# Performance work log

Hardware: AMD Instinct MI355X
Metric: run time of the kernel (lower is better)

## Reference

```python
import jax, jax.numpy as jnp
import numpy as np

B, S, D, E, K = 4, 2048, 2048, 64, 2

def setup_inputs() -> dict:
    key = jax.random.key(0)
    k1, k2, k3, k4 = jax.random.split(key, 4)
    x = jax.random.normal(k1, (B, S, D), dtype=jnp.float32)
    W = jax.random.normal(k2, (E, D), dtype=jnp.float32) * 0.02  # gate_linear.weight
    noise_weight = jax.random.normal(k3, (E,), dtype=jnp.float32) * 0.02
    noise = jax.random.normal(k4, (B, S, E), dtype=jnp.float32)  # torch.randn_like(logits), noisy_std=1.0
    return {"x": x, "W": W, "noise_weight": noise_weight, "noise": noise, "k": K}

def reference(x, W, noise_weight, noise, k):
    # logits = x @ W.T  -> [B, S, E]
    logits = jnp.einsum('bsd,ed->bse', x, W)
    # noise injection: randn * noisy_std(=1.0) * noise_weight (per-expert scale)
    logits_noisy = logits + noise * noise_weight
    # top-k over experts
    top_vals, top_idx = jax.lax.top_k(logits_noisy, k)  # [B, S, k]
    # softmax over a tensor that is -inf everywhere except the top-k slots is
    # exactly: zeros everywhere, softmax(top_vals) scattered into the top-k slots.
    probs = jax.nn.softmax(top_vals, axis=-1)  # [B, S, k]
    n_tok = B * S
    rows = jnp.arange(n_tok)[:, None]  # [n_tok, 1]
    gated = jnp.zeros((n_tok, E), dtype=logits.dtype)
    gated = gated.at[rows, top_idx.reshape(n_tok, k)].set(probs.reshape(n_tok, k))
    gated = gated.reshape(B, S, E)
    return gated, top_idx, top_vals
```

## Files before the change

kernel.cpp:

```cpp
#include <hip/hip_runtime.h>
#include <math.h>

#define NTOK 8192
#define DDIM 2048
#define NEXP 64
#define MT   16
#define BK   256
#define NCH  (DDIM / BK)
#define XSTR 264
#define CSTR 66

typedef _Float16 f16x8 __attribute__((ext_vector_type(8)));
typedef float    f32x4 __attribute__((ext_vector_type(4)));

#define GATED_SZ (NTOK * NEXP)
#define IDX_OFF  GATED_SZ
#define VALS_OFF (GATED_SZ + NTOK * 2)

#define NKSTEP (DDIM / 32)
#define NTILE  (NEXP / 16)
#define BFRAG_HALVES ((size_t)NKSTEP * NTILE * 64 * 8)

__global__ void pack_b_kernel(const float* __restrict__ W,
                              _Float16* __restrict__ Bh,
                              _Float16* __restrict__ Bl)
{
    const int tid  = blockIdx.x * blockDim.x + threadIdx.x;
    const int lane = tid & 63;
    const int fid  = tid >> 6;
    const int ks   = fid >> 2;
    const int nt   = fid & 3;
    const int e    = nt * 16 + (lane & 15);
    const int k    = ks * 32 + (lane >> 4) * 8;
    const float* src = W + (size_t)e * DDIM + k;

    f16x8 hi, lo;
#pragma unroll
    for (int j = 0; j < 8; ++j) {
        const float v = src[j];
        const _Float16 h = (_Float16)v;
        hi[j] = h;
        lo[j] = (_Float16)((v - (float)h) * 4096.f);
    }
    *(f16x8*)(Bh + (size_t)tid * 8) = hi;
    *(f16x8*)(Bl + (size_t)tid * 8) = lo;
}

#define BFRAG(base, ks) (*(const f16x8*)((base) + ((((size_t)(ks)) * 4 + nt) * 64 + lane) * 8))

__global__ __launch_bounds__(512, 4) void gate_kernel(
    const float* __restrict__ x,
    const _Float16* __restrict__ Bh,
    const _Float16* __restrict__ Bl,
    const float* __restrict__ noise_w,
    const float* __restrict__ noise,
    float* __restrict__ out)
{
    __shared__ _Float16 xh[2][MT * XSTR];
    __shared__ _Float16 xl[2][MT * XSTR];
    __shared__ float    cbuf[2][MT * CSTR];

    const int tid  = threadIdx.x;
    const int lane = tid & 63;
    const int w    = __builtin_amdgcn_readfirstlane(tid >> 6);
    const int h    = w >> 2;
    const int nt   = w & 3;
    const int tokBase = blockIdx.x * MT;

    const int srow = tid >> 5;
    const int scol = tid & 31;
    const float* xsrc = x + (size_t)(tokBase + srow) * DDIM + scol * 8;

    const int q = lane >> 4;
    const int m = lane & 15;
    const int abase = m * XSTR + h * (BK / 2) + q * 8;

    f32x4 acc_hh = {0.f, 0.f, 0.f, 0.f};
    f32x4 acc_lo = {0.f, 0.f, 0.f, 0.f};

    float4 st0 = *(const float4*)(xsrc);
    float4 st1 = *(const float4*)(xsrc + 4);

    for (int c = 0; c < NCH; ++c) {
        const int p = c & 1;

        {
            f16x8 h8, l8;
            const float vv[8] = {st0.x, st0.y, st0.z, st0.w,
                                 st1.x, st1.y, st1.z, st1.w};
#pragma unroll
            for (int j = 0; j < 8; ++j) {
                const _Float16 hh = (_Float16)vv[j];
                h8[j] = hh;
                l8[j] = (_Float16)((vv[j] - (float)hh) * 4096.f);
            }
            *(f16x8*)&xh[p][srow * XSTR + scol * 8] = h8;
            *(f16x8*)&xl[p][srow * XSTR + scol * 8] = l8;
        }

        if (c + 1 < NCH) {
            st0 = *(const float4*)(xsrc + (size_t)(c + 1) * BK);
            st1 = *(const float4*)(xsrc + (size_t)(c + 1) * BK + 4);
        }

        __syncthreads();

        const int ksb = c * 8 + h * 4;
#pragma unroll
        for (int stp = 0; stp < 4; ++stp) {
            const f16x8 bh = BFRAG(Bh, ksb + stp);
            const f16x8 bl = BFRAG(Bl, ksb + stp);
            const f16x8 ah = *(const f16x8*)&xh[p][abase + stp * 32];
            const f16x8 al = *(const f16x8*)&xl[p][abase + stp * 32];
            acc_hh = __builtin_amdgcn_mfma_f32_16x16x32_f16(ah, bh, acc_hh, 0, 0, 0);
            acc_lo = __builtin_amdgcn_mfma_f32_16x16x32_f16(ah, bl, acc_lo, 0, 0, 0);
            acc_lo = __builtin_amdgcn_mfma_f32_16x16x32_f16(al, bh, acc_lo, 0, 0, 0);
        }
    }

    {
        const int e = nt * 16 + m;
#pragma unroll
        for (int r = 0; r < 4; ++r) {
            const int t = q * 4 + r;
            cbuf[h][t * CSTR + e] = acc_hh[r] + acc_lo[r] * (1.f / 4096.f);
        }
    }
    __syncthreads();

    const float nwv = noise_w[lane];
#pragma unroll
    for (int i = 0; i < 2; ++i) {
        const int t   = w * 2 + i;
        const int tok = tokBase + t;
        const int e   = lane;

        float v = cbuf[0][t * CSTR + e] + cbuf[1][t * CSTR + e]
                + noise[(size_t)tok * NEXP + e] * nwv;

        float m1 = v; int i1 = e;
#pragma unroll
        for (int sh = 32; sh > 0; sh >>= 1) {
            float ov = __shfl_xor(m1, sh, 64);
            int   oi = __shfl_xor(i1, sh, 64);
            if (ov > m1 || (ov == m1 && oi < i1)) { m1 = ov; i1 = oi; }
        }
        float vm = (e == i1) ? -INFINITY : v;
        float m2 = vm; int i2 = e;
#pragma unroll
        for (int sh = 32; sh > 0; sh >>= 1) {
            float ov = __shfl_xor(m2, sh, 64);
            int   oi = __shfl_xor(i2, sh, 64);
            if (ov > m2 || (ov == m2 && oi < i2)) { m2 = ov; i2 = oi; }
        }

        const float e2  = expf(m2 - m1);
        const float inv = 1.f / (1.f + e2);
        const float p1  = inv;
        const float p2  = e2 * inv;

        float gval = 0.f;
        if (e == i1) gval = p1;
        else if (e == i2) gval = p2;
        out[(size_t)tok * NEXP + e] = gval;

        if (lane == 0) {
            out[IDX_OFF  + tok * 2 + 0] = (float)i1;
            out[IDX_OFF  + tok * 2 + 1] = (float)i2;
            out[VALS_OFF + tok * 2 + 0] = m1;
            out[VALS_OFF + tok * 2 + 1] = m2;
        }
    }
}

extern "C" void kernel_launch(void* const* d_in, const int* in_sizes, int n_in,
                              void* d_out, int out_size, void* d_ws, size_t ws_size,
                              hipStream_t stream) {
    const float* x      = (const float*)d_in[0];
    const float* W      = (const float*)d_in[1];
    const float* nw     = (const float*)d_in[2];
    const float* noise  = (const float*)d_in[3];
    float* out = (float*)d_out;

    _Float16* Bh = (_Float16*)d_ws;
    _Float16* Bl = Bh + BFRAG_HALVES;

    hipLaunchKernelGGL(pack_b_kernel, dim3(64), dim3(256), 0, stream, W, Bh, Bl);

    hipLaunchKernelGGL(gate_kernel, dim3(NTOK / MT), dim3(512), 0, stream,
                       x, Bh, Bl, nw, noise, out);
}
```

Before: 112.5 us.

## Split K across two blocks with atomic-counter reduction of partial logits

Splits the 2048-long reduction across two separate 256-thread blocks per 16-token group, replacing the old split across two halves inside one 512-thread block. Each block writes its partial logits to a workspace buffer and bumps an atomic counter. The second block to arrive adds its partner's partial and does the noise, top-2 and softmax epilogue. This doubles the block count and shrinks per-block LDS to raise occupancy, at the cost of extra global traffic for partials, fences, and a counter reset in the pack kernel.

```diff
diff --git a/kernel.cpp b/kernel.cpp
--- a/kernel.cpp
+++ b/kernel.cpp
@@ -5,10 +5,13 @@
 #define DDIM 2048
 #define NEXP 64
 #define MT   16
-#define BK   256
-#define NCH  (DDIM / BK)
-#define XSTR 264
-#define CSTR 66
+#define KSPL 2
+#define KSLC (DDIM / KSPL)
+#define BK   128
+#define NCH  (KSLC / BK)
+#define XSTR 136
+#define CSTR 68
+#define NGRP (NTOK / MT)
 
 typedef _Float16 f16x8 __attribute__((ext_vector_type(8)));
 typedef float    f32x4 __attribute__((ext_vector_type(4)));
@@ -21,11 +24,18 @@
 #define NTILE  (NEXP / 16)
 #define BFRAG_HALVES ((size_t)NKSTEP * NTILE * 64 * 8)
 
+#define P_OFF_FLOATS  (2 * BFRAG_HALVES / 2)
+#define P_FLOATS_PER  (MT * NEXP)
+#define CNT_OFF_INTS  (131072 + KSPL * NGRP * P_FLOATS_PER)
+
 __global__ void pack_b_kernel(const float* __restrict__ W,
                               _Float16* __restrict__ Bh,
-                              _Float16* __restrict__ Bl)
+                              _Float16* __restrict__ Bl,
+                              int* __restrict__ cnt)
 {
     const int tid  = blockIdx.x * blockDim.x + threadIdx.x;
+    if (tid < NGRP) cnt[tid] = 0;
+
     const int lane = tid & 63;
     const int fid  = tid >> 6;
     const int ks   = fid >> 2;
@@ -46,34 +56,38 @@
     *(f16x8*)(Bl + (size_t)tid * 8) = lo;
 }
 
-#define BFRAG(base, ks) (*(const f16x8*)((base) + ((((size_t)(ks)) * 4 + nt) * 64 + lane) * 8))
-
-__global__ __launch_bounds__(512, 4) void gate_kernel(
+#define BFRAG(base, kstep) \
+    (*(const f16x8*)((base) + ((((size_t)(kstep)) * 4 + nt) * 64 + lane) * 8))
+
+__global__ __launch_bounds__(256, 6) void gate_kernel(
     const float* __restrict__ x,
     const _Float16* __restrict__ Bh,
     const _Float16* __restrict__ Bl,
     const float* __restrict__ noise_w,
     const float* __restrict__ noise,
+    float* __restrict__ P,
+    int* __restrict__ cnt,
     float* __restrict__ out)
 {
-    __shared__ _Float16 xh[2][MT * XSTR];
-    __shared__ _Float16 xl[2][MT * XSTR];
-    __shared__ float    cbuf[2][MT * CSTR];
+    __shared__ _Float16 pool[2][2][MT * XSTR];
+    __shared__ int sflag;
+    float* cbuf = (float*)pool;
 
     const int tid  = threadIdx.x;
     const int lane = tid & 63;
     const int w    = __builtin_amdgcn_readfirstlane(tid >> 6);
-    const int h    = w >> 2;
-    const int nt   = w & 3;
-    const int tokBase = blockIdx.x * MT;
-
-    const int srow = tid >> 5;
-    const int scol = tid & 31;
-    const float* xsrc = x + (size_t)(tokBase + srow) * DDIM + scol * 8;
+    const int nt   = w;
+    const int grp  = blockIdx.x >> 1;
+    const int ks   = blockIdx.x & 1;
+    const int tokBase = grp * MT;
+
+    const int srow = tid >> 4;
+    const int scol = tid & 15;
+    const float* xsrc = x + (size_t)(tokBase + srow) * DDIM + ks * KSLC + scol * 8;
 
     const int q = lane >> 4;
     const int m = lane & 15;
-    const int abase = m * XSTR + h * (BK / 2) + q * 8;
+    const int abase = m * XSTR + q * 8;
 
     f32x4 acc_hh = {0.f, 0.f, 0.f, 0.f};
     f32x4 acc_lo = {0.f, 0.f, 0.f, 0.f};
@@ -94,8 +108,8 @@
                 h8[j] = hh;
                 l8[j] = (_Float16)((vv[j] - (float)hh) * 4096.f);
             }
-            *(f16x8*)&xh[p][srow * XSTR + scol * 8] = h8;
-            *(f16x8*)&xl[p][srow * XSTR + scol * 8] = l8;
+            *(f16x8*)&pool[p][0][srow * XSTR + scol * 8] = h8;
+            *(f16x8*)&pool[p][1][srow * XSTR + scol * 8] = l8;
         }
 
         if (c + 1 < NCH) {
@@ -105,37 +119,54 @@
 
         __syncthreads();
 
-        const int ksb = c * 8 + h * 4;
+        const int ksb = ks * 32 + c * 4;
 #pragma unroll
         for (int stp = 0; stp < 4; ++stp) {
             const f16x8 bh = BFRAG(Bh, ksb + stp);
             const f16x8 bl = BFRAG(Bl, ksb + stp);
-            const f16x8 ah = *(const f16x8*)&xh[p][abase + stp * 32];
-            const f16x8 al = *(const f16x8*)&xl[p][abase + stp * 32];
+            const f16x8 ah = *(const f16x8*)&pool[p][0][abase + stp * 32];
+            const f16x8 al = *(const f16x8*)&pool[p][1][abase + stp * 32];
             acc_hh = __builtin_amdgcn_mfma_f32_16x16x32_f16(ah, bh, acc_hh, 0, 0, 0);
             acc_lo = __builtin_amdgcn_mfma_f32_16x16x32_f16(ah, bl, acc_lo, 0, 0, 0);
             acc_lo = __builtin_amdgcn_mfma_f32_16x16x32_f16(al, bh, acc_lo, 0, 0, 0);
         }
     }
 
+    __syncthreads();
+
     {
         const int e = nt * 16 + m;
 #pragma unroll
         for (int r = 0; r < 4; ++r) {
             const int t = q * 4 + r;
-            cbuf[h][t * CSTR + e] = acc_hh[r] + acc_lo[r] * (1.f / 4096.f);
+            cbuf[t * CSTR + e] = acc_hh[r] + acc_lo[r] * (1.f / 4096.f);
         }
     }
     __syncthreads();
 
+    {
+        const int t  = tid >> 4;
+        const int e0 = (tid & 15) * 4;
+        float* dst = P + ((size_t)ks * NGRP + grp) * P_FLOATS_PER + t * NEXP + e0;
+        *(float4*)dst = *(float4*)&cbuf[t * CSTR + e0];
+    }
+    __threadfence();
+    if (tid == 0)
+        sflag = (atomicAdd(&cnt[grp], 1) == 1);
+    __syncthreads();
+    if (!sflag) return;
+    __threadfence();
+
+    const float* partner = P + ((size_t)(ks ^ 1) * NGRP + grp) * P_FLOATS_PER;
+
     const float nwv = noise_w[lane];
 #pragma unroll
-    for (int i = 0; i < 2; ++i) {
-        const int t   = w * 2 + i;
+    for (int i = 0; i < 4; ++i) {
+        const int t   = w * 4 + i;
         const int tok = tokBase + t;
         const int e   = lane;
 
-        float v = cbuf[0][t * CSTR + e] + cbuf[1][t * CSTR + e]
+        float v = cbuf[t * CSTR + e] + partner[t * NEXP + e]
                 + noise[(size_t)tok * NEXP + e] * nwv;
 
         float m1 = v; int i1 = e;
@@ -184,9 +215,12 @@
 
     _Float16* Bh = (_Float16*)d_ws;
     _Float16* Bl = Bh + BFRAG_HALVES;
-
-    hipLaunchKernelGGL(pack_b_kernel, dim3(64), dim3(256), 0, stream, W, Bh, Bl);
-
-    hipLaunchKernelGGL(gate_kernel, dim3(NTOK / MT), dim3(512), 0, stream,
-                       x, Bh, Bl, nw, noise, out);
+    float*    P  = (float*)d_ws + 131072;
+    int*      cnt = (int*)((float*)d_ws + CNT_OFF_INTS);
+
+    hipLaunchKernelGGL(pack_b_kernel, dim3(64), dim3(256), 0, stream,
+                       W, Bh, Bl, cnt);
+
+    hipLaunchKernelGGL(gate_kernel, dim3(NGRP * KSPL), dim3(256), 0, stream,
+                       x, Bh, Bl, nw, noise, P, cnt, out);
 }
```

New measurement: 320.7 us. 185% more time.
